# Kernel optimization log

Measured on AMD Instinct MI355X. Metric: run time of the kernel, lower is better.

The kernel has to match this reference:

```python
import jax, jax.numpy as jnp
import numpy as np

FEAT_DIM = 2048
HIDDEN = 1024
ATTN_DIM = 512
BATCH = 128
NPOS = 196


def setup_inputs() -> dict:
    key = jax.random.key(0)
    ks = jax.random.split(key, 8)
    # Linear layers use kaiming-uniform-ish init; plain scaled normal is fine for a numeric baseline.
    def lin(k, fan_in, fan_out):
        k1, k2 = jax.random.split(k)
        bound = 1.0 / np.sqrt(fan_in)
        W = jax.random.uniform(k1, (fan_out, fan_in), jnp.float32, -bound, bound)
        b = jax.random.uniform(k2, (fan_out,), jnp.float32, -bound, bound)
        return W, b
    We, be = lin(ks[0], FEAT_DIM, ATTN_DIM)
    Wd, bd = lin(ks[1], HIDDEN, ATTN_DIM)
    Wf, bf = lin(ks[2], ATTN_DIM, 1)
    encoder_out = jax.random.normal(ks[3], (BATCH, NPOS, FEAT_DIM), jnp.float32)
    hidden = jax.random.normal(ks[4], (BATCH, HIDDEN), jnp.float32)
    return {
        "encoder_out": encoder_out,
        "hidden": hidden,
        "We": We, "be": be,
        "Wd": Wd, "bd": bd,
        "Wf": Wf, "bf": bf,
    }


def reference(encoder_out, hidden, We, be, Wd, bd, Wf, bf):
    # enc: [B, P, A]; dec: [B, 1, A]
    enc = jnp.einsum('bpf,af->bpa', encoder_out, We) + be
    dec = (jnp.einsum('bh,ah->ba', hidden, Wd) + bd)[:, None, :]
    scores = jnp.tanh(enc + dec)
    # full_attn: [A] -> scalar per position; Wf has shape [1, A]
    scores = jnp.einsum('bpa,a->bp', scores, Wf[0]) + bf[0]
    alpha = jax.nn.softmax(scores, axis=1)  # [B, P]
    context = jnp.einsum('bpf,bp->bf', encoder_out, alpha)  # [B, F]
    return context, alpha
```

## Files before the change

kernel.cpp:

```cpp
#include <hip/hip_runtime.h>
#include <hip/hip_bf16.h>

typedef __bf16 bf16x8 __attribute__((ext_vector_type(8)));
typedef float f32x4 __attribute__((ext_vector_type(4)));

#define FEAT 2048
#define HID  1024
#define AD   512
#define NB   128
#define NP   196
#define MROWS (NB * NP)
#define BM 64
#define BK 64
#define NSTEP (FEAT / BK)
#define NBLK (MROWS / BM * 2)

__global__ __launch_bounds__(256) void pack_we_k(const float* __restrict__ We,
                                                 __bf16* __restrict__ Bp) {
    int t = blockIdx.x * 256 + threadIdx.x;
    int a  = t >> 8;
    int f0 = (t & 255) << 3;
    const float4* src = reinterpret_cast<const float4*>(We + ((size_t)a << 11) + f0);
    float4 x0 = src[0], x1 = src[1];
    int nt = a >> 4, r = a & 15;
    int kt = f0 >> 5, g = (f0 >> 3) & 3;
    size_t off = (((size_t)(kt * 32 + nt) * 64) + (r + (g << 4))) << 3;
    union { __bf16 h[8]; bf16x8 v; } u;
    u.h[0] = (__bf16)x0.x; u.h[1] = (__bf16)x0.y; u.h[2] = (__bf16)x0.z; u.h[3] = (__bf16)x0.w;
    u.h[4] = (__bf16)x1.x; u.h[5] = (__bf16)x1.y; u.h[6] = (__bf16)x1.z; u.h[7] = (__bf16)x1.w;
    *reinterpret_cast<bf16x8*>(Bp + off) = u.v;
}

__global__ __launch_bounds__(256) void dec_k(const float* __restrict__ hidden,
                                             const float* __restrict__ Wd,
                                             const float* __restrict__ bd,
                                             const float* __restrict__ be,
                                             float* __restrict__ decb) {
    __shared__ float w[8][1028];
    const int tid = threadIdx.x;
    const int n0 = blockIdx.x << 3;
    const float4* wsrc = reinterpret_cast<const float4*>(Wd + ((size_t)n0 << 10));
    #pragma unroll
    for (int i = 0; i < 8; ++i)
        *reinterpret_cast<float4*>(&w[i][tid << 2]) = wsrc[(i << 8) + tid];
    __syncthreads();
    const int nl = tid & 7, b0 = tid >> 3;
    float acc[4] = {0.f, 0.f, 0.f, 0.f};
    const float4* wp = reinterpret_cast<const float4*>(&w[nl][0]);
    #pragma unroll 2
    for (int k4 = 0; k4 < 256; ++k4) {
        float4 wv = wp[k4];
        #pragma unroll
        for (int i = 0; i < 4; ++i) {
            const float4 h = reinterpret_cast<const float4*>(
                hidden + ((size_t)(b0 + (i << 5)) << 10))[k4];
            acc[i] = fmaf(wv.x, h.x, acc[i]);
            acc[i] = fmaf(wv.y, h.y, acc[i]);
            acc[i] = fmaf(wv.z, h.z, acc[i]);
            acc[i] = fmaf(wv.w, h.w, acc[i]);
        }
    }
    const float bias = bd[n0 + nl] + be[n0 + nl];
    #pragma unroll
    for (int i = 0; i < 4; ++i)
        decb[(size_t)(b0 + (i << 5)) * AD + n0 + nl] = acc[i] + bias;
}

__device__ __forceinline__ void store16(char* d0, char* d1,
                                        float4 a, float4 b, float4 c, float4 d) {
    union { __bf16 h[8]; bf16x8 v; } u0, u1;
    u0.h[0]=(__bf16)a.x; u0.h[1]=(__bf16)a.y; u0.h[2]=(__bf16)a.z; u0.h[3]=(__bf16)a.w;
    u0.h[4]=(__bf16)b.x; u0.h[5]=(__bf16)b.y; u0.h[6]=(__bf16)b.z; u0.h[7]=(__bf16)b.w;
    u1.h[0]=(__bf16)c.x; u1.h[1]=(__bf16)c.y; u1.h[2]=(__bf16)c.z; u1.h[3]=(__bf16)c.w;
    u1.h[4]=(__bf16)d.x; u1.h[5]=(__bf16)d.y; u1.h[6]=(__bf16)d.z; u1.h[7]=(__bf16)d.w;
    *reinterpret_cast<bf16x8*>(d0) = u0.v;
    *reinterpret_cast<bf16x8*>(d1) = u1.v;
}

__device__ __forceinline__ void do_step(const char* buf, const __bf16* __restrict__ bs,
                                        int rc0, int rc1, int lr, f32x4 acc[4][4]) {
    #pragma unroll
    for (int kt2 = 0; kt2 < 2; ++kt2) {
        const __bf16* bk = bs + kt2 * 16384;
        bf16x8 b0 = *reinterpret_cast<const bf16x8*>(bk);
        bf16x8 b1 = *reinterpret_cast<const bf16x8*>(bk + 512);
        bf16x8 b2 = *reinterpret_cast<const bf16x8*>(bk + 1024);
        bf16x8 b3 = *reinterpret_cast<const bf16x8*>(bk + 1536);
        const int rc = kt2 ? rc1 : rc0;
        #pragma unroll
        for (int mt = 0; mt < 4; ++mt) {
            bf16x8 a = *reinterpret_cast<const bf16x8*>(buf + (mt * 16 + lr) * 128 + rc);
            acc[mt][0] = __builtin_amdgcn_mfma_f32_16x16x32_bf16(a, b0, acc[mt][0], 0, 0, 0);
            acc[mt][1] = __builtin_amdgcn_mfma_f32_16x16x32_bf16(a, b1, acc[mt][1], 0, 0, 0);
            acc[mt][2] = __builtin_amdgcn_mfma_f32_16x16x32_bf16(a, b2, acc[mt][2], 0, 0, 0);
            acc[mt][3] = __builtin_amdgcn_mfma_f32_16x16x32_bf16(a, b3, acc[mt][3], 0, 0, 0);
        }
    }
}

__global__ __launch_bounds__(256, 3) void enc_score_k(
        const float* __restrict__ X, const __bf16* __restrict__ Bp,
        const float* __restrict__ decb, const float* __restrict__ Wf,
        float* __restrict__ spart) {
    __shared__ char ldsA0[BM * BK * 2];
    __shared__ char ldsA1[BM * BK * 2];
    __shared__ float swave[4][BM];
    const int tid  = threadIdx.x;
    const int wave = tid >> 6, lane = tid & 63;
    const int lr = lane & 15, lg = lane >> 4;
    const int vbid = (blockIdx.x & 7) * (NBLK / 8) + (blockIdx.x >> 3);
    const int rt = vbid >> 1, nh = vbid & 1;
    const int row0 = rt * BM;
    const int ncol0 = nh * 256 + wave * 64;

    f32x4 acc[4][4];
    #pragma unroll
    for (int mt = 0; mt < 4; ++mt) {
        #pragma unroll
        for (int j = 0; j < 4; ++j) {
            const int row = mt * 16 + lg * 4 + j;
            const int b = (unsigned)(row0 + row) / 196u;
            const float* dp = decb + (size_t)b * AD + ncol0 + lr;
            #pragma unroll
            for (int nt = 0; nt < 4; ++nt) acc[mt][nt][j] = dp[nt * 16];
        }
    }

    const int srow = tid >> 2, sq = tid & 3;
    const float* gA = X + (size_t)(row0 + srow) * FEAT + sq * 16;
    const int swz = (srow & 7) << 4;
    char* wp0a = ldsA0 + srow * 128 + ((sq * 32) ^ swz);
    char* wp0b = ldsA0 + srow * 128 + ((sq * 32 + 16) ^ swz);
    char* wp1a = ldsA1 + srow * 128 + ((sq * 32) ^ swz);
    char* wp1b = ldsA1 + srow * 128 + ((sq * 32 + 16) ^ swz);

    const int rswz = (lr & 7) << 4;
    const int rc0 = (lg * 16) ^ rswz;
    const int rc1 = (64 + lg * 16) ^ rswz;
    const __bf16* bbase = Bp + (size_t)(nh * 16 + wave * 4) * 512 + lane * 8;

    float4 rA0, rA1, rA2, rA3, rB0, rB1, rB2, rB3;
    {   const float4* g = reinterpret_cast<const float4*>(gA);
        rA0 = g[0]; rA1 = g[1]; rA2 = g[2]; rA3 = g[3]; }
    store16(wp0a, wp0b, rA0, rA1, rA2, rA3);
    {   const float4* g = reinterpret_cast<const float4*>(gA + 64);
        rB0 = g[0]; rB1 = g[1]; rB2 = g[2]; rB3 = g[3]; }

    for (int s = 0; s < NSTEP; s += 2) {
        const bool more = (s + 2 < NSTEP);
        __syncthreads();
        if (more) {
            const float4* g = reinterpret_cast<const float4*>(gA + (size_t)(s + 2) * BK);
            rA0 = g[0]; rA1 = g[1]; rA2 = g[2]; rA3 = g[3];
        }
        do_step(ldsA0, bbase + (size_t)s * 32768, rc0, rc1, lr, acc);
        store16(wp1a, wp1b, rB0, rB1, rB2, rB3);
        __syncthreads();
        if (more) {
            const float4* g = reinterpret_cast<const float4*>(gA + (size_t)(s + 3) * BK);
            rB0 = g[0]; rB1 = g[1]; rB2 = g[2]; rB3 = g[3];
        }
        do_step(ldsA1, bbase + (size_t)(s + 1) * 32768, rc0, rc1, lr, acc);
        if (more) store16(wp0a, wp0b, rA0, rA1, rA2, rA3);
    }

    float wf[4];
    #pragma unroll
    for (int nt = 0; nt < 4; ++nt) wf[nt] = Wf[ncol0 + nt * 16 + lr];
    #pragma unroll
    for (int mt = 0; mt < 4; ++mt) {
        #pragma unroll
        for (int j = 0; j < 4; ++j) {
            float s = 0.f;
            #pragma unroll
            for (int nt = 0; nt < 4; ++nt) {
                float x = acc[mt][nt][j];
                float e = __expf(2.0f * x);
                float t = 1.0f - 2.0f / (e + 1.0f);
                s = fmaf(t, wf[nt], s);
            }
            s += __shfl_xor(s, 1); s += __shfl_xor(s, 2);
            s += __shfl_xor(s, 4); s += __shfl_xor(s, 8);
            if (lr == 0) swave[wave][mt * 16 + lg * 4 + j] = s;
        }
    }
    __syncthreads();
    if (tid < BM) {
        float s = swave[0][tid] + swave[1][tid] + swave[2][tid] + swave[3][tid];
        spart[(size_t)nh * MROWS + row0 + tid] = s;
    }
}

__global__ __launch_bounds__(64) void softmax_k(const float* __restrict__ spart,
                                                float* __restrict__ alpha) {
    const int b = blockIdx.x, lane = threadIdx.x;
    float v[4], e[4];
    float m = -3.0e38f;
    #pragma unroll
    for (int i = 0; i < 4; ++i) {
        int p = i * 64 + lane;
        v[i] = (p < NP) ? (spart[b * NP + p] + spart[MROWS + b * NP + p]) : -3.0e38f;
        m = fmaxf(m, v[i]);
    }
    #pragma unroll
    for (int o = 1; o < 64; o <<= 1) m = fmaxf(m, __shfl_xor(m, o));
    float s = 0.f;
    #pragma unroll
    for (int i = 0; i < 4; ++i) {
        int p = i * 64 + lane;
        e[i] = (p < NP) ? __expf(v[i] - m) : 0.f;
        s += e[i];
    }
    #pragma unroll
    for (int o = 1; o < 64; o <<= 1) s += __shfl_xor(s, o);
    const float inv = 1.0f / s;
    #pragma unroll
    for (int i = 0; i < 4; ++i) {
        int p = i * 64 + lane;
        if (p < NP) alpha[b * NP + p] = e[i] * inv;
    }
}

__global__ __launch_bounds__(128) void context_k(const float* __restrict__ X,
                                                 const float* __restrict__ alpha,
                                                 float* __restrict__ ctx) {
    __shared__ float al[NP];
    const int bid = blockIdx.x;
    const int b = 127 - (bid >> 2);
    const int chunk = bid & 3;
    const int tid = threadIdx.x;
    for (int i = tid; i < NP; i += 128) al[i] = alpha[b * NP + i];
    __syncthreads();
    const float4* Xp = reinterpret_cast<const float4*>(X + (size_t)b * NP * FEAT)
                       + chunk * 128 + tid;
    float4 a0 = {0,0,0,0}, a1 = {0,0,0,0};
    #pragma unroll 4
    for (int p = 0; p < NP; p += 2) {
        const float w0 = al[p], w1 = al[p + 1];
        const float4 x0 = Xp[(size_t)p * 512];
        const float4 x1 = Xp[(size_t)(p + 1) * 512];
        a0.x = fmaf(w0, x0.x, a0.x); a0.y = fmaf(w0, x0.y, a0.y);
        a0.z = fmaf(w0, x0.z, a0.z); a0.w = fmaf(w0, x0.w, a0.w);
        a1.x = fmaf(w1, x1.x, a1.x); a1.y = fmaf(w1, x1.y, a1.y);
        a1.z = fmaf(w1, x1.z, a1.z); a1.w = fmaf(w1, x1.w, a1.w);
    }
    float4 r; r.x = a0.x + a1.x; r.y = a0.y + a1.y; r.z = a0.z + a1.z; r.w = a0.w + a1.w;
    *reinterpret_cast<float4*>(ctx + (size_t)b * FEAT + chunk * 512 + tid * 4) = r;
}

extern "C" void kernel_launch(void* const* d_in, const int* in_sizes, int n_in,
                              void* d_out, int out_size, void* d_ws, size_t ws_size,
                              hipStream_t stream) {
    const float* enc    = (const float*)d_in[0];
    const float* hidden = (const float*)d_in[1];
    const float* We     = (const float*)d_in[2];
    const float* be     = (const float*)d_in[3];
    const float* Wd     = (const float*)d_in[4];
    const float* bd     = (const float*)d_in[5];
    const float* Wf     = (const float*)d_in[6];

    float* out   = (float*)d_out;
    float* ctx   = out;
    float* alpha = out + NB * FEAT;

    char* ws = (char*)d_ws;
    __bf16* Bp    = (__bf16*)ws;
    float*  decb  = (float*)(ws + (2u << 20));
    float*  spart = (float*)(ws + (2u << 20) + (256u << 10));

    pack_we_k  <<<dim3(512), dim3(256), 0, stream>>>(We, Bp);
    dec_k      <<<dim3(64),  dim3(256), 0, stream>>>(hidden, Wd, bd, be, decb);
    enc_score_k<<<dim3(NBLK), dim3(256), 0, stream>>>(enc, Bp, decb, Wf, spart);
    softmax_k  <<<dim3(NB),  dim3(64),  0, stream>>>(spart, alpha);
    context_k  <<<dim3(512), dim3(128), 0, stream>>>(enc, alpha, ctx);
}
```

Baseline: 192.8 us.

## Retile encoder GEMM to 128x128 blocks with LDS-staged B via global_load_lds

Changes the encoder-score GEMM tile from 64 rows by 256 columns to 128 rows by 128 columns, using a 2x2 wave layout. The B operand is now staged through double-buffered LDS with async global_load_lds, where before each wave read it directly from global memory. A is now single-buffered in LDS with register prefetch. The goal is better reuse of the weight tiles and fewer redundant global B reads. In exchange, four partial score buffers must be summed in softmax, there is more LDS per block, and the single A buffer brings extra barriers.

New measurement: 242.3 us. +25.6%, slower.

```diff
diff --git a/kernel.cpp b/kernel.cpp
--- a/kernel.cpp
+++ b/kernel.cpp
@@ -10,10 +10,17 @@
 #define NB   128
 #define NP   196
 #define MROWS (NB * NP)
-#define BM 64
+#define BM 128
+#define BN 128
 #define BK 64
 #define NSTEP (FEAT / BK)
-#define NBLK (MROWS / BM * 2)
+#define NBLK (MROWS / BM * 4)
+
+__device__ __forceinline__ void gload16(const void* g, void* l) {
+    __builtin_amdgcn_global_load_lds(
+        (const __attribute__((address_space(1))) void*)(g),
+        (__attribute__((address_space(3))) void*)(l), 16, 0, 0);
+}
 
 __global__ __launch_bounds__(256) void pack_we_k(const float* __restrict__ We,
                                                  __bf16* __restrict__ Bp) {
@@ -66,59 +73,28 @@
         decb[(size_t)(b0 + (i << 5)) * AD + n0 + nl] = acc[i] + bias;
 }
 
-__device__ __forceinline__ void store16(char* d0, char* d1,
-                                        float4 a, float4 b, float4 c, float4 d) {
-    union { __bf16 h[8]; bf16x8 v; } u0, u1;
-    u0.h[0]=(__bf16)a.x; u0.h[1]=(__bf16)a.y; u0.h[2]=(__bf16)a.z; u0.h[3]=(__bf16)a.w;
-    u0.h[4]=(__bf16)b.x; u0.h[5]=(__bf16)b.y; u0.h[6]=(__bf16)b.z; u0.h[7]=(__bf16)b.w;
-    u1.h[0]=(__bf16)c.x; u1.h[1]=(__bf16)c.y; u1.h[2]=(__bf16)c.z; u1.h[3]=(__bf16)c.w;
-    u1.h[4]=(__bf16)d.x; u1.h[5]=(__bf16)d.y; u1.h[6]=(__bf16)d.z; u1.h[7]=(__bf16)d.w;
-    *reinterpret_cast<bf16x8*>(d0) = u0.v;
-    *reinterpret_cast<bf16x8*>(d1) = u1.v;
-}
-
-__device__ __forceinline__ void do_step(const char* buf, const __bf16* __restrict__ bs,
-                                        int rc0, int rc1, int lr, f32x4 acc[4][4]) {
-    #pragma unroll
-    for (int kt2 = 0; kt2 < 2; ++kt2) {
-        const __bf16* bk = bs + kt2 * 16384;
-        bf16x8 b0 = *reinterpret_cast<const bf16x8*>(bk);
-        bf16x8 b1 = *reinterpret_cast<const bf16x8*>(bk + 512);
-        bf16x8 b2 = *reinterpret_cast<const bf16x8*>(bk + 1024);
-        bf16x8 b3 = *reinterpret_cast<const bf16x8*>(bk + 1536);
-        const int rc = kt2 ? rc1 : rc0;
-        #pragma unroll
-        for (int mt = 0; mt < 4; ++mt) {
-            bf16x8 a = *reinterpret_cast<const bf16x8*>(buf + (mt * 16 + lr) * 128 + rc);
-            acc[mt][0] = __builtin_amdgcn_mfma_f32_16x16x32_bf16(a, b0, acc[mt][0], 0, 0, 0);
-            acc[mt][1] = __builtin_amdgcn_mfma_f32_16x16x32_bf16(a, b1, acc[mt][1], 0, 0, 0);
-            acc[mt][2] = __builtin_amdgcn_mfma_f32_16x16x32_bf16(a, b2, acc[mt][2], 0, 0, 0);
-            acc[mt][3] = __builtin_amdgcn_mfma_f32_16x16x32_bf16(a, b3, acc[mt][3], 0, 0, 0);
-        }
-    }
-}
-
 __global__ __launch_bounds__(256, 3) void enc_score_k(
         const float* __restrict__ X, const __bf16* __restrict__ Bp,
         const float* __restrict__ decb, const float* __restrict__ Wf,
         float* __restrict__ spart) {
-    __shared__ char ldsA0[BM * BK * 2];
-    __shared__ char ldsA1[BM * BK * 2];
-    __shared__ float swave[4][BM];
+    __shared__ char Asm[BM * BK * 2];
+    __shared__ char Bsm[2][16384];
+    __shared__ float swave[2][BM];
     const int tid  = threadIdx.x;
     const int wave = tid >> 6, lane = tid & 63;
     const int lr = lane & 15, lg = lane >> 4;
-    const int vbid = (blockIdx.x & 7) * (NBLK / 8) + (blockIdx.x >> 3);
-    const int rt = vbid >> 1, nh = vbid & 1;
+    const int wm = wave >> 1, wn = wave & 1;
+    const int vbid = (blockIdx.x & 7) * 98 + (blockIdx.x >> 3);
+    const int rt = vbid >> 2, nq = vbid & 3;
     const int row0 = rt * BM;
-    const int ncol0 = nh * 256 + wave * 64;
+    const int ncol0 = nq * BN + wn * 64;
 
     f32x4 acc[4][4];
     #pragma unroll
     for (int mt = 0; mt < 4; ++mt) {
         #pragma unroll
         for (int j = 0; j < 4; ++j) {
-            const int row = mt * 16 + lg * 4 + j;
+            const int row = wm * 64 + mt * 16 + lg * 4 + j;
             const int b = (unsigned)(row0 + row) / 196u;
             const float* dp = decb + (size_t)b * AD + ncol0 + lr;
             #pragma unroll
@@ -126,42 +102,92 @@
         }
     }
 
-    const int srow = tid >> 2, sq = tid & 3;
-    const float* gA = X + (size_t)(row0 + srow) * FEAT + sq * 16;
+    const int srow = tid >> 1, sq = tid & 1;
+    const float* gA = X + (size_t)(row0 + srow) * FEAT + sq * 32;
     const int swz = (srow & 7) << 4;
-    char* wp0a = ldsA0 + srow * 128 + ((sq * 32) ^ swz);
-    char* wp0b = ldsA0 + srow * 128 + ((sq * 32 + 16) ^ swz);
-    char* wp1a = ldsA1 + srow * 128 + ((sq * 32) ^ swz);
-    char* wp1b = ldsA1 + srow * 128 + ((sq * 32 + 16) ^ swz);
+    char* awr = Asm + srow * 128;
+
+    const char* BpB = (const char*)Bp;
+    const int c0 = wave * 4;
+    int csrc[4];
+    #pragma unroll
+    for (int i = 0; i < 4; ++i) {
+        const int c = c0 + i;
+        csrc[i] = (c >> 3) * 32 + nq * 8 + (c & 7);
+    }
 
     const int rswz = (lr & 7) << 4;
-    const int rc0 = (lg * 16) ^ rswz;
-    const int rc1 = (64 + lg * 16) ^ rswz;
-    const __bf16* bbase = Bp + (size_t)(nh * 16 + wave * 4) * 512 + lane * 8;
-
-    float4 rA0, rA1, rA2, rA3, rB0, rB1, rB2, rB3;
-    {   const float4* g = reinterpret_cast<const float4*>(gA);
-        rA0 = g[0]; rA1 = g[1]; rA2 = g[2]; rA3 = g[3]; }
-    store16(wp0a, wp0b, rA0, rA1, rA2, rA3);
-    {   const float4* g = reinterpret_cast<const float4*>(gA + 64);
-        rB0 = g[0]; rB1 = g[1]; rB2 = g[2]; rB3 = g[3]; }
-
-    for (int s = 0; s < NSTEP; s += 2) {
-        const bool more = (s + 2 < NSTEP);
-        __syncthreads();
-        if (more) {
-            const float4* g = reinterpret_cast<const float4*>(gA + (size_t)(s + 2) * BK);
-            rA0 = g[0]; rA1 = g[1]; rA2 = g[2]; rA3 = g[3];
-        }
-        do_step(ldsA0, bbase + (size_t)s * 32768, rc0, rc1, lr, acc);
-        store16(wp1a, wp1b, rB0, rB1, rB2, rB3);
-        __syncthreads();
-        if (more) {
-            const float4* g = reinterpret_cast<const float4*>(gA + (size_t)(s + 3) * BK);
-            rB0 = g[0]; rB1 = g[1]; rB2 = g[2]; rB3 = g[3];
-        }
-        do_step(ldsA1, bbase + (size_t)(s + 1) * 32768, rc0, rc1, lr, acc);
-        if (more) store16(wp0a, wp0b, rA0, rA1, rA2, rA3);
+
+    float4 r[8];
+    {
+        const float4* g = reinterpret_cast<const float4*>(gA);
+        #pragma unroll
+        for (int i = 0; i < 8; ++i) r[i] = g[i];
+    }
+    #pragma unroll
+    for (int i = 0; i < 4; ++i)
+        gload16(BpB + ((size_t)(csrc[i] << 6) + lane) * 16, Bsm[0] + (c0 + i) * 1024);
+    #pragma unroll
+    for (int u = 0; u < 4; ++u) {
+        union { __bf16 h[8]; bf16x8 v; } p;
+        p.h[0]=(__bf16)r[2*u].x; p.h[1]=(__bf16)r[2*u].y; p.h[2]=(__bf16)r[2*u].z; p.h[3]=(__bf16)r[2*u].w;
+        p.h[4]=(__bf16)r[2*u+1].x; p.h[5]=(__bf16)r[2*u+1].y; p.h[6]=(__bf16)r[2*u+1].z; p.h[7]=(__bf16)r[2*u+1].w;
+        *reinterpret_cast<bf16x8*>(awr + ((sq * 64 + u * 16) ^ swz)) = p.v;
+    }
+    {
+        const float4* g = reinterpret_cast<const float4*>(gA + 64);
+        #pragma unroll
+        for (int i = 0; i < 8; ++i) r[i] = g[i];
+    }
+    asm volatile("s_waitcnt vmcnt(8) lgkmcnt(0)" ::: "memory");
+    __builtin_amdgcn_s_barrier();
+
+    int cur = 0;
+    for (int t = 0; t < NSTEP; ++t) {
+        if (t < NSTEP - 1) {
+            const size_t kbase = (size_t)(2 * (t + 1)) * 32 * 1024;
+            #pragma unroll
+            for (int i = 0; i < 4; ++i)
+                gload16(BpB + kbase + ((size_t)(csrc[i] << 6) + lane) * 16,
+                        Bsm[cur ^ 1] + (c0 + i) * 1024);
+        }
+        #pragma unroll
+        for (int kt2 = 0; kt2 < 2; ++kt2) {
+            bf16x8 bfr[4];
+            #pragma unroll
+            for (int j = 0; j < 4; ++j)
+                bfr[j] = *reinterpret_cast<const bf16x8*>(
+                    Bsm[cur] + ((kt2 * 8 + wn * 4 + j) * 64 + lane) * 16);
+            #pragma unroll
+            for (int mt = 0; mt < 4; ++mt) {
+                bf16x8 a = *reinterpret_cast<const bf16x8*>(
+                    Asm + (wm * 64 + mt * 16 + lr) * 128 + ((kt2 * 64 + lg * 16) ^ rswz));
+                acc[mt][0] = __builtin_amdgcn_mfma_f32_16x16x32_bf16(a, bfr[0], acc[mt][0], 0, 0, 0);
+                acc[mt][1] = __builtin_amdgcn_mfma_f32_16x16x32_bf16(a, bfr[1], acc[mt][1], 0, 0, 0);
+                acc[mt][2] = __builtin_amdgcn_mfma_f32_16x16x32_bf16(a, bfr[2], acc[mt][2], 0, 0, 0);
+                acc[mt][3] = __builtin_amdgcn_mfma_f32_16x16x32_bf16(a, bfr[3], acc[mt][3], 0, 0, 0);
+            }
+        }
+        if (t < NSTEP - 1) {
+            __builtin_amdgcn_s_barrier();
+            #pragma unroll
+            for (int u = 0; u < 4; ++u) {
+                union { __bf16 h[8]; bf16x8 v; } p;
+                p.h[0]=(__bf16)r[2*u].x; p.h[1]=(__bf16)r[2*u].y; p.h[2]=(__bf16)r[2*u].z; p.h[3]=(__bf16)r[2*u].w;
+                p.h[4]=(__bf16)r[2*u+1].x; p.h[5]=(__bf16)r[2*u+1].y; p.h[6]=(__bf16)r[2*u+1].z; p.h[7]=(__bf16)r[2*u+1].w;
+                *reinterpret_cast<bf16x8*>(awr + ((sq * 64 + u * 16) ^ swz)) = p.v;
+            }
+            if (t < NSTEP - 2) {
+                const float4* g = reinterpret_cast<const float4*>(gA + (size_t)(t + 2) * BK);
+                #pragma unroll
+                for (int i = 0; i < 8; ++i) r[i] = g[i];
+                asm volatile("s_waitcnt vmcnt(8) lgkmcnt(0)" ::: "memory");
+            } else {
+                asm volatile("s_waitcnt vmcnt(0) lgkmcnt(0)" ::: "memory");
+            }
+            __builtin_amdgcn_s_barrier();
+            cur ^= 1;
+        }
     }
 
     float wf[4];
@@ -181,14 +207,12 @@
             }
             s += __shfl_xor(s, 1); s += __shfl_xor(s, 2);
             s += __shfl_xor(s, 4); s += __shfl_xor(s, 8);
-            if (lr == 0) swave[wave][mt * 16 + lg * 4 + j] = s;
+            if (lr == 0) swave[wn][wm * 64 + mt * 16 + lg * 4 + j] = s;
         }
     }
     __syncthreads();
-    if (tid < BM) {
-        float s = swave[0][tid] + swave[1][tid] + swave[2][tid] + swave[3][tid];
-        spart[(size_t)nh * MROWS + row0 + tid] = s;
-    }
+    if (tid < BM)
+        spart[(size_t)nq * MROWS + row0 + tid] = swave[0][tid] + swave[1][tid];
 }
 
 __global__ __launch_bounds__(64) void softmax_k(const float* __restrict__ spart,
@@ -199,7 +223,11 @@
     #pragma unroll
     for (int i = 0; i < 4; ++i) {
         int p = i * 64 + lane;
-        v[i] = (p < NP) ? (spart[b * NP + p] + spart[MROWS + b * NP + p]) : -3.0e38f;
+        if (p < NP) {
+            int idx = b * NP + p;
+            v[i] = spart[idx] + spart[MROWS + idx] + spart[2 * MROWS + idx]
+                 + spart[3 * MROWS + idx];
+        } else v[i] = -3.0e38f;
         m = fmaxf(m, v[i]);
     }
     #pragma unroll
@@ -244,8 +272,8 @@
         a1.x = fmaf(w1, x1.x, a1.x); a1.y = fmaf(w1, x1.y, a1.y);
         a1.z = fmaf(w1, x1.z, a1.z); a1.w = fmaf(w1, x1.w, a1.w);
     }
-    float4 r; r.x = a0.x + a1.x; r.y = a0.y + a1.y; r.z = a0.z + a1.z; r.w = a0.w + a1.w;
-    *reinterpret_cast<float4*>(ctx + (size_t)b * FEAT + chunk * 512 + tid * 4) = r;
+    float4 rr; rr.x = a0.x + a1.x; rr.y = a0.y + a1.y; rr.z = a0.z + a1.z; rr.w = a0.w + a1.w;
+    *reinterpret_cast<float4*>(ctx + (size_t)b * FEAT + chunk * 512 + tid * 4) = rr;
 }
 
 extern "C" void kernel_launch(void* const* d_in, const int* in_sizes, int n_in,
```
